# Kernel optimization log

Measured on AMD Instinct MI355X. Metric: run time of the kernel, lower is better.

The kernel has to match this reference:

```python
import jax, jax.numpy as jnp
import numpy as np

B, L, D = 4, 256, 1024
D4 = D // 4
K = 3          # conv kernel size
NL = 3         # num conv layers
MAXLEN = 500   # relative-encoding max_len
R = 8          # rel_types


def _make_pe():
    # sinusoidal table over positions max_len .. -max_len (torch buffer 'pe')
    position = MAXLEN - np.arange(2 * MAXLEN + 1)
    div = np.exp(np.arange(0, D, 2) * (-np.log(10000.0) / D))
    vals = position[:, None] * div[None, :]
    pe = np.zeros((2 * MAXLEN + 1, D), dtype=np.float32)
    pe[:, 0::2] = np.sin(vals)
    pe[:, 1::2] = np.cos(vals)
    return jnp.asarray(pe)

PE = _make_pe()  # constant buffer, (2*max_len+1, D)


def _ln(x, eps=1e-5):
    mu = x.mean(-1, keepdims=True)
    v = ((x - mu) ** 2).mean(-1, keepdims=True)
    return (x - mu) * jax.lax.rsqrt(v + eps)


def setup_inputs() -> dict:
    key = jax.random.key(0)
    ks = jax.random.split(key, 16)
    X = jax.random.normal(ks[0], (B, L, D), jnp.float32)
    lengths = jax.random.randint(ks[1], (B,), L // 2, L + 1)
    mask = jnp.arange(L)[None, :] < lengths[:, None]  # True = valid token
    s = lambda fan: 1.0 / np.sqrt(fan)
    conv_w = jax.random.normal(ks[2], (NL, D, D, K), jnp.float32) * s(D * K)
    conv_b = jnp.zeros((NL, D), jnp.float32)
    Wc = jax.random.normal(ks[3], (D4, D), jnp.float32) * s(D)
    bc = jnp.zeros((D4,), jnp.float32)
    Wp = jax.random.normal(ks[4], (D4, D), jnp.float32) * s(D)
    bp = jnp.zeros((D4,), jnp.float32)
    Wcum = jax.random.normal(ks[5], (D4, D), jnp.float32) * s(D)
    bcum = jnp.zeros((D4,), jnp.float32)
    Wr = jax.random.normal(ks[6], (D4, D), jnp.float32) * s(D)
    br = jnp.zeros((D4,), jnp.float32)
    ln_g = jnp.ones((D4,), jnp.float32)
    ln_b = jnp.zeros((D4,), jnp.float32)
    Wo = jax.random.normal(ks[7], (R, D4), jnp.float32) * 0.05  # zeros at init; use small random for a nontrivial baseline
    bo = jnp.zeros((R,), jnp.float32)
    return {"X": X, "conv_w": conv_w, "conv_b": conv_b, "Wc": Wc, "bc": bc,
            "Wp": Wp, "bp": bp, "Wcum": Wcum, "bcum": bcum, "Wr": Wr, "br": br,
            "ln_g": ln_g, "ln_b": ln_b, "Wo": Wo, "bo": bo, "mask": mask}


def reference(X, conv_w, conv_b, Wc, bc, Wp, bp, Wcum, bcum, Wr, br,
              ln_g, ln_b, Wo, bo, mask):
    vis = mask[:, :, None] & mask[:, None, :]  # (B,L,L)

    # cumulative projection of the raw input (computed before the conv stack)
    cum = jnp.einsum('bld,kd->blk', X, Wcum) + bcum            # (B,L,D4)
    cum = jnp.where(mask[..., None], 0.0, cum)                 # masked_fill(mask, 0) as in source
    cumul_h = jnp.pad(jnp.cumsum(cum, axis=1), ((0, 0), (1, 0), (0, 0)))  # (B,L+1,D4)
    f_cumul = cumul_h[:, :-1]                                   # (B,L,D4)
    b_cumul = cumul_h[:, -1:, :] - cumul_h[:, 1:]               # (B,L,D4)
    cumul_lin = f_cumul[:, :, None, :] - b_cumul[:, None, :, :]  # (B,L,L,D4)

    # conv sequence processor (eval mode: dropout = identity)
    h = X
    for i in range(NL):
        h_in = jnp.where(mask[..., None], h, 0.0)
        xc = jnp.transpose(h_in, (0, 2, 1))                     # (B,D,L)
        yc = jax.lax.conv_general_dilated(
            xc, conv_w[i], window_strides=(1,), padding=[(1, 1)],
            dimension_numbers=('NCH', 'OIH', 'NCH'))
        y = jnp.transpose(yc, (0, 2, 1)) + conv_b[i]            # (B,L,D)
        h = jnp.tanh(_ln(y))                                     # LayerNorm (no affine) + Tanh

    c_lin = h @ Wc.T + bc                                        # (B,L,D4)
    p_lin = h @ Wp.T + bp                                        # (B,L,D4)

    # relative positional scores: relpos[i,j] = transform(pe[max_len + i - j])
    pos = PE @ Wr.T + br                                         # (2*max_len+1, D4)
    idx = MAXLEN + jnp.arange(L)[:, None] - jnp.arange(L)[None, :]
    relpos = pos[idx]                                            # (L,L,D4)

    hid = c_lin[:, :, None, :] + p_lin[:, None, :, :] + cumul_lin + relpos[None]
    hid = jnp.tanh(_ln(hid) * ln_g + ln_b)                       # LayerNorm(affine) + Tanh

    logits = jnp.tanh((hid @ Wo.T + bo) / 7.5) * 7.5             # (B,L,L,R)
    logits = jnp.where(vis[..., None], logits, -64.0)
    root = jnp.transpose(jnp.diagonal(logits, axis1=1, axis2=2), (0, 2, 1))  # (B,L,R)
    return logits, root, h
```

## Files before the change

### kernel.cpp

```cpp
#include <hip/hip_runtime.h>

#define B_ 4
#define L_ 256
#define D_ 1024
#define D4_ 256
#define R_ 8

typedef __attribute__((ext_vector_type(8))) __bf16 bf16x8;
typedef __attribute__((ext_vector_type(4))) __bf16 bf16x4;
typedef __attribute__((ext_vector_type(4))) float f32x4;
typedef __attribute__((ext_vector_type(2))) float f32x2;

__device__ __forceinline__ float4 ld4(const float* p){ return *reinterpret_cast<const float4*>(p); }
__device__ __forceinline__ void st4(float* p, float4 v){ *reinterpret_cast<float4*>(p) = v; }

__device__ __forceinline__ float fast_tanh(float x){
  x = fminf(fmaxf(x, -9.f), 9.f);
  float e = exp2f(x * 2.885390081777927f);
  return (e - 1.f) * __builtin_amdgcn_rcpf(e + 1.f);
}

__device__ __forceinline__ f32x2 fast_tanh2(f32x2 x){
  const f32x2 kk = {2.885390081777927f, 2.885390081777927f};
  f32x2 kx = x * kk;
  float c0 = fminf(fmaxf(kx[0], -26.f), 26.f);
  float c1 = fminf(fmaxf(kx[1], -26.f), 26.f);
  f32x2 e = { exp2f(c0), exp2f(c1) };
  f32x2 den = e + (f32x2){1.f, 1.f};
  f32x2 r = { __builtin_amdgcn_rcpf(den[0]), __builtin_amdgcn_rcpf(den[1]) };
  return (f32x2){-2.f, -2.f} * r + (f32x2){1.f, 1.f};
}

__device__ __forceinline__ int mask_stride(const unsigned char* mask){
  const unsigned int* w = (const unsigned int*)mask;
  unsigned int w0 = w[0];
  if (w0 == 0x01010101u) return 1;
  if (w0 == 0x3F803F80u) return 2;
  if (w0 == 0x3C003C00u) return 2;
  if (w0 == 0x3F800000u) return 4;
  if (w0 == 1u) return (w[1] == 1u) ? 4 : 8;
  if (w0 == 0u && w[1] == 0x3FF00000u) return 8;
  return 1;
}
__device__ __forceinline__ bool mask_at(const unsigned char* mask, int stride, int idx){
  const unsigned char* e = mask + (size_t)idx * stride;
  unsigned char nz = 0;
  for (int s = 0; s < stride; s++) nz |= e[s];
  return nz != 0;
}

__global__ __launch_bounds__(256) void k_megaprep(
    const float* __restrict__ X, const unsigned char* __restrict__ mask,
    __bf16* __restrict__ xu, __bf16* __restrict__ xm,
    const float* __restrict__ cw, __bf16* __restrict__ wbc,
    const float* __restrict__ w0, const float* __restrict__ w1,
    const float* __restrict__ w2, const float* __restrict__ w3,
    __bf16* __restrict__ o0, __bf16* __restrict__ o1,
    __bf16* __restrict__ o2, __bf16* __restrict__ o3,
    __bf16* __restrict__ pe,
    const float* __restrict__ Wo, float* __restrict__ wot)
{
  int blk = blockIdx.x, tid = threadIdx.x;
  if (blk < 512){
    int idx = blk*256 + tid;
    int row = idx >> 7, c8 = (idx & 127) << 3;
    int stride = mask_stride(mask);
    bool keep = mask_at(mask, stride, row);
    const float* src = X + ((size_t)row << 10) + c8;
    bf16x8 u, m;
    #pragma unroll
    for (int e = 0; e < 8; e++){
      float f = src[e];
      u[e] = (__bf16)f;
      m[e] = keep ? (__bf16)f : (__bf16)0.f;
    }
    *reinterpret_cast<bf16x8*>(xu + ((size_t)row<<10) + c8) = u;
    *reinterpret_cast<bf16x8*>(xm + ((size_t)row<<10) + c8) = m;
  } else if (blk < 1024){
    int sub = blk - 512;
    const float* src; __bf16* dst;
    switch (sub >> 7){
      case 0: src = w0; dst = o0; break;
      case 1: src = w1; dst = o1; break;
      case 2: src = w2; dst = o2; break;
      default: src = w3; dst = o3; break;
    }
    int idx = (sub & 127)*256 + tid;
    const float* p = src + (size_t)idx*8;
    bf16x8 v;
    #pragma unroll
    for (int e = 0; e < 8; e++) v[e] = (__bf16)p[e];
    *reinterpret_cast<bf16x8*>(dst + (size_t)idx*8) = v;
  } else if (blk < 4096){
    int idx = (blk - 1024)*256 + tid;
    int layer = idx / 262144;
    int rem = idx & 262143;
    int o = rem >> 8, c4 = (rem & 255) << 2;
    const float* src = cw + (((size_t)layer*1024 + o)*1024 + c4)*3;
    float4 f0 = ld4(src), f1 = ld4(src+4), f2 = ld4(src+8);
    float tv[3][4] = {
      {f0.x, f0.w, f1.z, f2.y},
      {f0.y, f1.x, f1.w, f2.z},
      {f0.z, f1.y, f2.x, f2.w}
    };
    #pragma unroll
    for (int t = 0; t < 3; t++){
      bf16x4 v;
      #pragma unroll
      for (int e = 0; e < 4; e++) v[e] = (__bf16)tv[t][e];
      *reinterpret_cast<bf16x4*>(wbc + ((size_t)(layer*3+t)*1024 + o)*1024 + c4) = v;
    }
  } else if (blk < 4607){
    int t = blk - 4096;
    float posv = (float)(255 - t);
    const float c = -9.210340371976184f / (float)D_;
    for (int m = tid; m < D_/2; m += 256){
      float div = __expf((float)(2*m) * c);
      float val = posv * div;
      pe[((size_t)t<<10) + 2*m]     = (__bf16)__sinf(val);
      pe[((size_t)t<<10) + 2*m + 1] = (__bf16)__cosf(val);
    }
  } else {
    for (int e = tid; e < 2048; e += 256)
      wot[e] = Wo[(((e >> 1) & 7) << 8) + ((e >> 4) << 1) + (e & 1)];
  }
}

__device__ __forceinline__ void gemm_body(__bf16 (*As)[64], __bf16 (*Bs)[64],
                                          const __bf16* __restrict__ A,
                                          const __bf16* __restrict__ Bw,
                                          const float* __restrict__ bias,
                                          const float* __restrict__ bias2,
                                          float* __restrict__ C,
                                          float* __restrict__ Ct,
                                          int M, int N, int Kd,
                                          int row0, int col0, int tid)
{
  int lane = tid & 63, wave = tid >> 6;
  int wv = __builtin_amdgcn_readfirstlane(wave);
  int wm = (wave >> 1) << 5, wn = (wave & 1) << 5;
  __bf16* as_flat = &As[0][0];
  __bf16* bs_flat = &Bs[0][0];
  bool safeA = (row0 + 64 <= M);
  f32x4 acc[2][2] = {};
  for (int k0 = 0; k0 < Kd; k0 += 64){
    if (safeA){
      #pragma unroll
      for (int it = 0; it < 2; it++){
        int sbase = (wv*2 + it) << 6;
        int s = sbase + lane;
        int r = s >> 3, cs = s & 7;
        const __bf16* gp = A + (size_t)(row0 + r)*Kd + k0 + ((cs ^ (r & 7)) << 3);
        __builtin_amdgcn_global_load_lds(gp, as_flat + ((size_t)sbase << 3), 16, 0, 0);
      }
    } else {
      for (int idx = tid; idx < 512; idx += 256){
        int r = idx >> 3, c = idx & 7;
        int row = row0 + r;
        bf16x8 v = {};
        if (row < M) v = *reinterpret_cast<const bf16x8*>(A + (size_t)row*Kd + k0 + (c<<3));
        *reinterpret_cast<bf16x8*>(&As[r][(c ^ (r & 7)) << 3]) = v;
      }
    }
    #pragma unroll
    for (int it = 0; it < 2; it++){
      int sbase = (wv*2 + it) << 6;
      int s = sbase + lane;
      int r = s >> 3, cs = s & 7;
      const __bf16* gp = Bw + (size_t)(col0 + r)*Kd + k0 + ((cs ^ (r & 7)) << 3);
      __builtin_amdgcn_global_load_lds(gp, bs_flat + ((size_t)sbase << 3), 16, 0, 0);
    }
    __syncthreads();
    #pragma unroll
    for (int kk = 0; kk < 2; kk++){
      int kc = (kk << 2) + (lane >> 4);
      int ra0 = wm + (lane & 15), ra1 = ra0 + 16;
      int rb0 = wn + (lane & 15), rb1 = rb0 + 16;
      bf16x8 a0 = *reinterpret_cast<const bf16x8*>(&As[ra0][(kc ^ (ra0 & 7)) << 3]);
      bf16x8 a1 = *reinterpret_cast<const bf16x8*>(&As[ra1][(kc ^ (ra1 & 7)) << 3]);
      bf16x8 b0 = *reinterpret_cast<const bf16x8*>(&Bs[rb0][(kc ^ (rb0 & 7)) << 3]);
      bf16x8 b1 = *reinterpret_cast<const bf16x8*>(&Bs[rb1][(kc ^ (rb1 & 7)) << 3]);
      acc[0][0] = __builtin_amdgcn_mfma_f32_16x16x32_bf16(a0, b0, acc[0][0], 0, 0, 0);
      acc[0][1] = __builtin_amdgcn_mfma_f32_16x16x32_bf16(a0, b1, acc[0][1], 0, 0, 0);
      acc[1][0] = __builtin_amdgcn_mfma_f32_16x16x32_bf16(a1, b0, acc[1][0], 0, 0, 0);
      acc[1][1] = __builtin_amdgcn_mfma_f32_16x16x32_bf16(a1, b1, acc[1][1], 0, 0, 0);
    }
    __syncthreads();
  }
  #pragma unroll
  for (int mi = 0; mi < 2; mi++)
    #pragma unroll
    for (int ni = 0; ni < 2; ni++){
      int col = col0 + wn + (ni << 4) + (lane & 15);
      float bv = bias ? ((col < 256) ? bias[col] : bias2[col - 256]) : 0.f;
      int rowb = row0 + wm + (mi << 4) + ((lane >> 4) << 2);
      if (Ct){
        float* dst = Ct + ((size_t)(col >> 2) << 11) + (col & 3);
        #pragma unroll
        for (int e = 0; e < 4; e++){
          int row = rowb + e;
          if (row < M) dst[row << 2] = acc[mi][ni][e] + bv;
        }
      } else {
        #pragma unroll
        for (int e = 0; e < 4; e++){
          int row = rowb + e;
          if (row < M) C[(size_t)row*N + col] = acc[mi][ni][e] + bv;
        }
      }
    }
}

__global__ __launch_bounds__(256) void k_gemm3(
    const __bf16* __restrict__ Xb_u, const __bf16* __restrict__ Wcum_b,
    const float* __restrict__ bcum, float* __restrict__ cum,
    const __bf16* __restrict__ hb_fin, const __bf16* __restrict__ Wc_b,
    const float* __restrict__ bc, const float* __restrict__ bp,
    float* __restrict__ cp_lin,
    const __bf16* __restrict__ pe_b, const __bf16* __restrict__ Wr_b,
    const float* __restrict__ br, float* __restrict__ pos_t)
{
  __shared__ __align__(16) __bf16 As[64][64];
  __shared__ __align__(16) __bf16 Bs[64][64];
  int blk = blockIdx.x, tid = threadIdx.x;
  if (blk < 64){
    gemm_body(As, Bs, Xb_u, Wcum_b, bcum, bcum, cum, nullptr,
              1024, 256, 1024, (blk & 15) << 6, (blk >> 4) << 6, tid);
  } else if (blk < 192){
    int s = blk - 64;
    gemm_body(As, Bs, hb_fin, Wc_b, bc, bp, cp_lin, nullptr,
              1024, 512, 1024, (s & 15) << 6, (s >> 4) << 6, tid);
  } else {
    int s = blk - 192;
    gemm_body(As, Bs, pe_b, Wr_b, br, br, nullptr, pos_t,
              511, 256, 1024, (s & 7) << 6, (s >> 3) << 6, tid);
  }
}

__global__ __launch_bounds__(256) void k_gemm_cross(
    const __bf16* __restrict__ ci_bf, const __bf16* __restrict__ pj_bf,
    const __bf16* __restrict__ pos_bf,
    float* __restrict__ G1, float* __restrict__ G2, float* __restrict__ G3)
{
  __shared__ __align__(16) __bf16 As[64][64];
  __shared__ __align__(16) __bf16 Bs[64][64];
  int blk = blockIdx.x, tid = threadIdx.x;
  if (blk < 64){
    int b = blk >> 4, s = blk & 15;
    gemm_body(As, Bs, ci_bf + ((size_t)b << 16), pj_bf + ((size_t)b << 16),
              nullptr, nullptr, G1 + ((size_t)b << 16), nullptr,
              256, 256, 256, (s & 3) << 6, (s >> 2) << 6, tid);
  } else if (blk < 192){
    int s = blk - 64;
    gemm_body(As, Bs, ci_bf, pos_bf, nullptr, nullptr, G2, nullptr,
              1024, 512, 256, (s & 15) << 6, (s >> 4) << 6, tid);
  } else {
    int s = blk - 192;
    gemm_body(As, Bs, pj_bf, pos_bf, nullptr, nullptr, G3, nullptr,
              1024, 512, 256, (s & 15) << 6, (s >> 4) << 6, tid);
  }
}

__global__ __launch_bounds__(256) void k_conv_mfma(const __bf16* __restrict__ hb,
                                                   const __bf16* __restrict__ wbc,
                                                   __bf16* __restrict__ y, int layer)
{
  __shared__ __align__(16) __bf16 As[66][64];
  __shared__ __align__(16) __bf16 Bs[3][64][64];
  int tid = threadIdx.x;
  int lane = tid & 63, wave = tid >> 6;
  int wv = __builtin_amdgcn_readfirstlane(wave);
  int wm = (wave >> 1) << 5, wn = (wave & 1) << 5;
  int n = blockIdx.x;
  int swz = (n & 7)*128 + (n >> 3);
  int bx = swz & 15, oy = (swz >> 4) & 15, z = swz >> 8;
  int b = bx >> 2, l0 = (bx & 3) << 6;
  int o0 = oy << 6;
  __bf16* as_flat = &As[0][0];
  __bf16* bs_flat = &Bs[0][0][0];
  f32x4 acc[2][2] = {};
  for (int cc = 0; cc < 4; cc++){
    int c0 = (z << 8) + (cc << 6);
    #pragma unroll
    for (int it = 0; it < 6; it++){
      int m = wv*6 + it;
      int s = (m << 6) + lane;
      int t = s >> 9, r = (s >> 3) & 63, c_ = s & 7;
      const __bf16* gp = wbc + ((size_t)((layer*3 + t) << 10) + o0 + r)*1024
                       + c0 + ((c_ ^ (r & 7)) << 3);
      __builtin_amdgcn_global_load_lds(gp, bs_flat + ((size_t)m << 9), 16, 0, 0);
    }
    #pragma unroll
    for (int it = 0; it < 2; it++){
      int sbase = (wv*2 + it) << 6;
      int s = sbase + lane;
      int r = 1 + (s >> 3), c = s & 7;
      const __bf16* gp = hb + (((size_t)(b<<8) + l0 - 1 + r) << 10)
                       + c0 + ((c ^ (r & 7)) << 3);
      __builtin_amdgcn_global_load_lds(gp, as_flat + 64 + ((size_t)sbase << 3), 16, 0, 0);
    }
    if (tid < 16){
      int rr = (tid >> 3) ? 65 : 0;
      int c = tid & 7;
      int l = l0 - 1 + rr;
      bf16x8 v = {};
      if (l >= 0 && l < L_)
        v = *reinterpret_cast<const bf16x8*>(hb + (((size_t)(b<<8) + l) << 10) + c0 + (c<<3));
      *reinterpret_cast<bf16x8*>(&As[rr][(c ^ (rr & 7)) << 3]) = v;
    }
    __syncthreads();
    #pragma unroll
    for (int t = 0; t < 3; t++){
      #pragma unroll
      for (int kk = 0; kk < 2; kk++){
        int kc = (kk << 2) + (lane >> 4);
        int ra0 = wm + (lane & 15) + t, ra1 = ra0 + 16;
        int rb0 = wn + (lane & 15),     rb1 = rb0 + 16;
        bf16x8 a0 = *reinterpret_cast<const bf16x8*>(&As[ra0][(kc ^ (ra0 & 7)) << 3]);
        bf16x8 a1 = *reinterpret_cast<const bf16x8*>(&As[ra1][(kc ^ (ra1 & 7)) << 3]);
        bf16x8 b0 = *reinterpret_cast<const bf16x8*>(&Bs[t][rb0][(kc ^ (rb0 & 7)) << 3]);
        bf16x8 b1 = *reinterpret_cast<const bf16x8*>(&Bs[t][rb1][(kc ^ (rb1 & 7)) << 3]);
        acc[0][0] = __builtin_amdgcn_mfma_f32_16x16x32_bf16(a0, b0, acc[0][0], 0, 0, 0);
        acc[0][1] = __builtin_amdgcn_mfma_f32_16x16x32_bf16(a0, b1, acc[0][1], 0, 0, 0);
        acc[1][0] = __builtin_amdgcn_mfma_f32_16x16x32_bf16(a1, b0, acc[1][0], 0, 0, 0);
        acc[1][1] = __builtin_amdgcn_mfma_f32_16x16x32_bf16(a1, b1, acc[1][1], 0, 0, 0);
      }
    }
    __syncthreads();
  }
  __bf16* yz = y + (size_t)z * 1048576;
  #pragma unroll
  for (int mi = 0; mi < 2; mi++)
    #pragma unroll
    for (int ni = 0; ni < 2; ni++){
      int col = o0 + wn + (ni << 4) + (lane & 15);
      #pragma unroll
      for (int e = 0; e < 4; e++){
        int rowl = wm + (mi << 4) + ((lane >> 4) << 2) + e;
        yz[(((size_t)(b<<8) + l0 + rowl) << 10) + col] = (__bf16)acc[mi][ni][e];
      }
    }
}

__device__ __forceinline__ void ln_core4(const __bf16* y, const float* cb, int n, int tid,
                                         int lane, int wid, float* red,
                                         float4& v, float& mu, float& rstd){
  const __bf16* yr = y + ((size_t)n << 10) + tid*4;
  bf16x4 a0 = *reinterpret_cast<const bf16x4*>(yr);
  bf16x4 a1 = *reinterpret_cast<const bf16x4*>(yr + 1048576);
  bf16x4 a2 = *reinterpret_cast<const bf16x4*>(yr + 2097152);
  bf16x4 a3 = *reinterpret_cast<const bf16x4*>(yr + 3145728);
  float4 bb = ld4(cb + tid*4);
  v = make_float4((float)a0[0]+(float)a1[0]+(float)a2[0]+(float)a3[0]+bb.x,
                  (float)a0[1]+(float)a1[1]+(float)a2[1]+(float)a3[1]+bb.y,
                  (float)a0[2]+(float)a1[2]+(float)a2[2]+(float)a3[2]+bb.z,
                  (float)a0[3]+(float)a1[3]+(float)a2[3]+(float)a3[3]+bb.w);
  float s = v.x+v.y+v.z+v.w;
  #pragma unroll
  for (int m=1;m<64;m<<=1) s += __shfl_xor(s, m);
  if (lane == 0) red[wid] = s;
  __syncthreads();
  mu = (red[0]+red[1]+red[2]+red[3]) * (1.f/D_);
  float d0=v.x-mu, d1=v.y-mu, d2=v.z-mu, d3=v.w-mu;
  float ss = d0*d0+d1*d1+d2*d2+d3*d3;
  #pragma unroll
  for (int m=1;m<64;m<<=1) ss += __shfl_xor(ss, m);
  if (lane == 0) red[8+wid] = ss;
  __syncthreads();
  rstd = rsqrtf((red[8]+red[9]+red[10]+red[11]) * (1.f/D_) + 1e-5f);
}

__global__ __launch_bounds__(256) void k_ln_tanh_mid(const __bf16* __restrict__ y,
                                                     const float* __restrict__ cb,
                                                     const unsigned char* __restrict__ mask,
                                                     __bf16* __restrict__ hb)
{
  __shared__ float red[16];
  int n = blockIdx.x;
  int tid = threadIdx.x, lane = tid & 63, wid = tid >> 6;
  float4 v; float mu, rstd;
  ln_core4(y, cb, n, tid, lane, wid, red, v, mu, rstd);
  int stride = mask_stride(mask);
  float keep = mask_at(mask, stride, n) ? 1.f : 0.f;
  bf16x4 o;
  o[0] = (__bf16)(fast_tanh((v.x-mu)*rstd) * keep);
  o[1] = (__bf16)(fast_tanh((v.y-mu)*rstd) * keep);
  o[2] = (__bf16)(fast_tanh((v.z-mu)*rstd) * keep);
  o[3] = (__bf16)(fast_tanh((v.w-mu)*rstd) * keep);
  *reinterpret_cast<bf16x4*>(hb + ((size_t)n<<10) + tid*4) = o;
}

__global__ __launch_bounds__(256) void k_ln_tanh_fin(const __bf16* __restrict__ y,
                                                     const float* __restrict__ cb,
                                                     float* __restrict__ hf,
                                                     __bf16* __restrict__ hb)
{
  __shared__ float red[16];
  int n = blockIdx.x;
  int tid = threadIdx.x, lane = tid & 63, wid = tid >> 6;
  float4 v; float mu, rstd;
  ln_core4(y, cb, n, tid, lane, wid, red, v, mu, rstd);
  float t0 = fast_tanh((v.x-mu)*rstd), t1 = fast_tanh((v.y-mu)*rstd);
  float t2 = fast_tanh((v.z-mu)*rstd), t3 = fast_tanh((v.w-mu)*rstd);
  st4(&hf[((size_t)n<<10) + tid*4], make_float4(t0,t1,t2,t3));
  bf16x4 o; o[0]=(__bf16)t0; o[1]=(__bf16)t1; o[2]=(__bf16)t2; o[3]=(__bf16)t3;
  *reinterpret_cast<bf16x4*>(hb + ((size_t)n<<10) + tid*4) = o;
}

__global__ __launch_bounds__(256) void k_combine(const float* __restrict__ cum,
                                                 const float* __restrict__ cp,
                                                 const unsigned char* __restrict__ mask,
                                                 float* __restrict__ ci,
                                                 float* __restrict__ pjt)
{
  __shared__ unsigned char mflag[256];
  int tid = threadIdx.x;
  int b = blockIdx.x >> 6;
  {
    int stride = mask_stride(mask);
    mflag[tid] = mask_at(mask, stride, (b << 8) + tid) ? 1 : 0;
  }
  __syncthreads();
  int w = blockIdx.x*4 + (tid >> 6);
  int lane = tid & 63;
  int k = w & 255;
  int rowbase = b << 8;
  float v[4], p[4];
  float run = 0.f;
  #pragma unroll
  for (int e = 0; e < 4; e++){
    int l = lane*4 + e;
    float x = cum[(((size_t)rowbase + l) << 8) + k];
    v[e] = mflag[l] ? 0.f : x;
    run += v[e]; p[e] = run;
  }
  float t = run, s = run;
  #pragma unroll
  for (int off = 1; off < 64; off <<= 1){
    float u = __shfl_up(s, off);
    if (lane >= off) s += u;
  }
  float excl = s - t;
  float total = __shfl(s, 63);
  float* pjb = pjt + (((size_t)((k >> 2)*4 + b)) << 10) + (k & 3);
  #pragma unroll
  for (int e = 0; e < 4; e++){
    int l = lane*4 + e;
    size_t row = rowbase + l;
    float f_ex = excl + p[e] - v[e];
    float b_in = total - (excl + p[e]);
    ci[(row << 8) + k] = cp[row*512 + k] + f_ex;
    pjb[l << 2] = cp[row*512 + 256 + k] - b_in;
  }
}

__global__ __launch_bounds__(256) void k_rowstats(const float* __restrict__ ci,
                                                  const float* __restrict__ pjt,
                                                  const float* __restrict__ post,
                                                  __bf16* __restrict__ ci_bf,
                                                  __bf16* __restrict__ pj_bf,
                                                  __bf16* __restrict__ pos_bf,
                                                  float* __restrict__ stats)
{
  int w = blockIdx.x*4 + (threadIdx.x >> 6);
  int lane = threadIdx.x & 63;
  float4 v; __bf16* dst; float* Sp; float* Qp;
  if (w < 1024){
    v = ld4(&ci[((size_t)w << 8) + (lane << 2)]);
    dst = ci_bf + ((size_t)w << 8) + (lane << 2);
    Sp = stats + w; Qp = stats + 1024 + w;
  } else if (w < 2048){
    int row = w - 1024;
    int b = row >> 8, j = row & 255;
    v = ld4(pjt + ((size_t)lane << 12) + (b << 10) + (j << 2));
    dst = pj_bf + ((size_t)row << 8) + (lane << 2);
    Sp = stats + 2048 + row; Qp = stats + 3072 + row;
  } else {
    int d = w - 2048;
    if (d < 511) v = ld4(post + ((size_t)lane << 11) + (d << 2));
    else         v = make_float4(0.f, 0.f, 0.f, 0.f);
    dst = pos_bf + ((size_t)d << 8) + (lane << 2);
    Sp = stats + 4096 + d; Qp = stats + 4608 + d;
  }
  bf16x4 o; o[0]=(__bf16)v.x; o[1]=(__bf16)v.y; o[2]=(__bf16)v.z; o[3]=(__bf16)v.w;
  *reinterpret_cast<bf16x4*>(dst) = o;
  float s = v.x+v.y+v.z+v.w;
  float qv = v.x*v.x + v.y*v.y + v.z*v.z + v.w*v.w;
  #pragma unroll
  for (int m = 1; m < 64; m <<= 1){
    s  += __shfl_xor(s,  m);
    qv += __shfl_xor(qv, m);
  }
  if (lane == 0){ *Sp = s; *Qp = qv; }
}

__global__ __launch_bounds__(256) void k_pairs(const float* __restrict__ ci,
                                               const float* __restrict__ pjt,
                                               const float* __restrict__ post,
                                               const float* __restrict__ ln_g,
                                               const float* __restrict__ ln_b,
                                               const float* __restrict__ wot,
                                               const float* __restrict__ bo,
                                               const unsigned char* __restrict__ mask,
                                               const float* __restrict__ stats,
                                               const float* __restrict__ G1,
                                               const float* __restrict__ G2,
                                               const float* __restrict__ G3,
                                               float* __restrict__ out)
{
  __shared__ float pacc[64][3][9];

  int bid = blockIdx.x;
  int qtr = bid & 3;
  int bi = bid >> 2;
  int b = bi >> 8, i = bi & 255;
  int tid = threadIdx.x;
  int jj = tid & 63, q = tid >> 6;
  int j = (qtr << 6) + jj;

  int d = i - j + 255;
  int bj = (b << 8) + j;
  const float* pjb = pjt + ((size_t)b << 10) + (j << 2);
  const float* pob = post + ((size_t)d << 2);
  const float* cbase = ci + ((size_t)bi << 8);
  int k40 = __builtin_amdgcn_readfirstlane(q << 4);

  float Sh = stats[bi] + stats[2048 + bj] + stats[4096 + d];
  float Qh = stats[1024 + bi] + stats[3072 + bj] + stats[4608 + d]
           + 2.f*(G1[((size_t)b << 16) + (i << 8) + j]
                + G2[((size_t)bi << 9) + d]
                + G3[((size_t)bj << 9) + d]);
  float mu = Sh * (1.f/256.f);
  float var = fmaxf(Qh * (1.f/256.f) - mu*mu, 0.f);
  float rstd = rsqrtf(var + 1e-5f);

  f32x2 aP0={0,0},aP1={0,0},aP2={0,0},aP3={0,0},aP4={0,0},aP5={0,0},aP6={0,0},aP7={0,0};
  f32x2 mmu = {-mu, -mu}, rr = {rstd, rstd};
  #pragma unroll 4
  for (int u = 0; u < 16; u++){
    int k4 = k40 + u;
    float4 c4 = ld4(cbase + (k4 << 2));
    float4 g4 = ld4(ln_g + (k4 << 2));
    float4 b4 = ld4(ln_b + (k4 << 2));
    float4 pv = ld4(pjb + ((size_t)k4 << 12));
    float4 ov = ld4(pob + ((size_t)k4 << 11));
    const float* wf = wot + (k4 << 5);
    float4 w0 = ld4(wf),      w1 = ld4(wf + 4);
    float4 w2 = ld4(wf + 8),  w3 = ld4(wf + 12);
    float4 w4 = ld4(wf + 16), w5 = ld4(wf + 20);
    float4 w6 = ld4(wf + 24), w7 = ld4(wf + 28);
    f32x2 hA = (f32x2){c4.x, c4.y} + (f32x2){pv.x, pv.y} + (f32x2){ov.x, ov.y};
    f32x2 hB = (f32x2){c4.z, c4.w} + (f32x2){pv.z, pv.w} + (f32x2){ov.z, ov.w};
    f32x2 gA = {g4.x, g4.y}, gB = {g4.z, g4.w};
    f32x2 bA = {b4.x, b4.y}, bB = {b4.z, b4.w};
    f32x2 argA = ((hA + mmu) * rr) * gA + bA;
    f32x2 argB = ((hB + mmu) * rr) * gB + bB;
    f32x2 vA = fast_tanh2(argA);
    f32x2 vB = fast_tanh2(argB);
    aP0 = vA * (f32x2){w0.x, w0.y} + aP0;  aP1 = vA * (f32x2){w0.z, w0.w} + aP1;
    aP2 = vA * (f32x2){w1.x, w1.y} + aP2;  aP3 = vA * (f32x2){w1.z, w1.w} + aP3;
    aP4 = vA * (f32x2){w2.x, w2.y} + aP4;  aP5 = vA * (f32x2){w2.z, w2.w} + aP5;
    aP6 = vA * (f32x2){w3.x, w3.y} + aP6;  aP7 = vA * (f32x2){w3.z, w3.w} + aP7;
    aP0 = vB * (f32x2){w4.x, w4.y} + aP0;  aP1 = vB * (f32x2){w4.z, w4.w} + aP1;
    aP2 = vB * (f32x2){w5.x, w5.y} + aP2;  aP3 = vB * (f32x2){w5.z, w5.w} + aP3;
    aP4 = vB * (f32x2){w6.x, w6.y} + aP4;  aP5 = vB * (f32x2){w6.z, w6.w} + aP5;
    aP6 = vB * (f32x2){w7.x, w7.y} + aP6;  aP7 = vB * (f32x2){w7.z, w7.w} + aP7;
  }
  float a0 = aP0[0]+aP0[1], a1 = aP1[0]+aP1[1];
  float a2 = aP2[0]+aP2[1], a3 = aP3[0]+aP3[1];
  float a4 = aP4[0]+aP4[1], a5 = aP5[0]+aP5[1];
  float a6 = aP6[0]+aP6[1], a7 = aP7[0]+aP7[1];
  if (q){
    float* pp = &pacc[jj][q-1][0];
    pp[0]=a0; pp[1]=a1; pp[2]=a2; pp[3]=a3;
    pp[4]=a4; pp[5]=a5; pp[6]=a6; pp[7]=a7;
  }
  __syncthreads();
  if (!q){
    const float* p0 = &pacc[jj][0][0];
    const float* p1 = &pacc[jj][1][0];
    const float* p2 = &pacc[jj][2][0];
    a0 += p0[0]+p1[0]+p2[0]; a1 += p0[1]+p1[1]+p2[1];
    a2 += p0[2]+p1[2]+p2[2]; a3 += p0[3]+p1[3]+p2[3];
    a4 += p0[4]+p1[4]+p2[4]; a5 += p0[5]+p1[5]+p2[5];
    a6 += p0[6]+p1[6]+p2[6]; a7 += p0[7]+p1[7]+p2[7];
    float acc[8] = {a0,a1,a2,a3,a4,a5,a6,a7};
    int stride = mask_stride(mask);
    bool vis = mask_at(mask, stride, bi) && mask_at(mask, stride, bj);
    float res[8];
    #pragma unroll
    for (int r = 0; r < 8; r++){
      float sc = (acc[r] + bo[r]) * (1.f/7.5f);
      res[r] = vis ? fast_tanh(sc)*7.5f : -64.f;
    }
    float* lp = out + (((size_t)bi << 8) + j)*8;
    st4(lp,     make_float4(res[0],res[1],res[2],res[3]));
    st4(lp + 4, make_float4(res[4],res[5],res[6],res[7]));
    if (j == i){
      float* rp = out + (size_t)B_*L_*L_*R_ + ((size_t)bi)*8;
      st4(rp,     make_float4(res[0],res[1],res[2],res[3]));
      st4(rp + 4, make_float4(res[4],res[5],res[6],res[7]));
    }
  }
}

extern "C" void kernel_launch(void* const* d_in, const int* in_sizes, int n_in,
                              void* d_out, int out_size, void* d_ws, size_t ws_size,
                              hipStream_t stream)
{
  const float* X      = (const float*)d_in[0];
  const float* conv_w = (const float*)d_in[1];
  const float* conv_b = (const float*)d_in[2];
  const float* Wc     = (const float*)d_in[3];
  const float* bc     = (const float*)d_in[4];
  const float* Wp     = (const float*)d_in[5];
  const float* bp     = (const float*)d_in[6];
  const float* Wcum   = (const float*)d_in[7];
  const float* bcum   = (const float*)d_in[8];
  const float* Wr     = (const float*)d_in[9];
  const float* br     = (const float*)d_in[10];
  const float* ln_g   = (const float*)d_in[11];
  const float* ln_b   = (const float*)d_in[12];
  const float* Wo     = (const float*)d_in[13];
  const float* bo     = (const float*)d_in[14];
  const unsigned char* mask = (const unsigned char*)d_in[15];
  float* out = (float*)d_out;

  char* base = (char*)d_ws;
  auto alloc = [&](size_t bytes){ char* p = base; base += (bytes + 255) & ~(size_t)255; return p; };
  __bf16* Xb_u    = (__bf16*)alloc(2097152);
  __bf16* Xb_m    = (__bf16*)alloc(2097152);
  __bf16* Wbc     = (__bf16*)alloc(18874368);
  __bf16* Wcum_b  = (__bf16*)alloc(524288);
  __bf16* Wc_b    = (__bf16*)alloc(524288);
  __bf16* Wp_b    = (__bf16*)alloc(524288);
  __bf16* Wr_b    = (__bf16*)alloc(524288);
  __bf16* pe_b    = (__bf16*)alloc(1046528);
  __bf16* ypart   = (__bf16*)alloc(8388608);
  __bf16* hb_mid  = (__bf16*)alloc(2097152);
  __bf16* hb_fin  = (__bf16*)alloc(2097152);
  float*  cum     = (float*) alloc(1048576);
  float*  cp_lin  = (float*) alloc(2097152);
  float*  ci_c    = (float*) alloc(1048576);
  float*  pj_t    = (float*) alloc(1048576);
  float*  pos_t   = (float*) alloc(524288);
  __bf16* ci_bf   = (__bf16*)alloc(524288);
  __bf16* pj_bf   = (__bf16*)alloc(524288);
  __bf16* pos_bf  = (__bf16*)alloc(262144);
  float*  statsB  = (float*) alloc(20480);
  float*  G1      = (float*) alloc(1048576);
  float*  G2      = (float*) alloc(2097152);
  float*  G3      = (float*) alloc(2097152);
  float*  wot     = (float*) alloc(8192);
  (void)Wp_b;

  float* h_out = out + (size_t)B_*L_*L_*R_ + (size_t)B_*L_*R_;

  k_megaprep<<<4608, 256, 0, stream>>>(X, mask, Xb_u, Xb_m, conv_w, Wbc,
                                       Wcum, Wc, Wp, Wr, Wcum_b, Wc_b, Wp_b, Wr_b,
                                       pe_b, Wo, wot);

  k_conv_mfma<<<1024, 256, 0, stream>>>(Xb_m,   Wbc, ypart, 0);
  k_ln_tanh_mid<<<B_*L_, 256, 0, stream>>>(ypart, conv_b,        mask, hb_mid);
  k_conv_mfma<<<1024, 256, 0, stream>>>(hb_mid, Wbc, ypart, 1);
  k_ln_tanh_mid<<<B_*L_, 256, 0, stream>>>(ypart, conv_b + 1024, mask, hb_mid);
  k_conv_mfma<<<1024, 256, 0, stream>>>(hb_mid, Wbc, ypart, 2);
  k_ln_tanh_fin<<<B_*L_, 256, 0, stream>>>(ypart, conv_b + 2048, h_out, hb_fin);

  k_gemm3<<<224, 256, 0, stream>>>(Xb_u, Wcum_b, bcum, cum,
                                   hb_fin, Wc_b, bc, bp, cp_lin,
                                   pe_b, Wr_b, br, pos_t);

  k_combine<<<256, 256, 0, stream>>>(cum, cp_lin, mask, ci_c, pj_t);

  k_rowstats<<<640, 256, 0, stream>>>(ci_c, pj_t, pos_t, ci_bf, pj_bf, pos_bf, statsB);
  k_gemm_cross<<<320, 256, 0, stream>>>(ci_bf, pj_bf, pos_bf, G1, G2, G3);

  k_pairs<<<B_*L_*4, 256, 0, stream>>>(ci_c, pj_t, pos_t, ln_g, ln_b, wot, bo,
                                       mask, statsB, G1, G2, G3, out);
}
```

Baseline: 148.2 us.

## Compute pair-hidden to logits projection with bf16 MFMA via LDS-staged tanh values

In k_pairs, each thread previously ran a scalar FMA projection of its tanh-activated hidden vector onto the 8 output weights, followed by an LDS reduction across four waves. Now the tanh outputs are packed to bf16 into a swizzled LDS tile (64 pairs by 256 features), and each wave runs 16x16x32 bf16 MFMAs against a zero-padded 16-row bf16 copy of Wo. This moves the dot products onto matrix cores and removes the partial-sum reduction. In exchange the activations and weights lose precision to bf16, half of the MFMA columns are padding, and the output stores become scalar per element.

After: 157.2 us. +6.1%, slower.

```diff
diff --git a/kernel.cpp b/kernel.cpp
--- a/kernel.cpp
+++ b/kernel.cpp
@@ -29,6 +29,13 @@
   f32x2 den = e + (f32x2){1.f, 1.f};
   f32x2 r = { __builtin_amdgcn_rcpf(den[0]), __builtin_amdgcn_rcpf(den[1]) };
   return (f32x2){-2.f, -2.f} * r + (f32x2){1.f, 1.f};
+}
+
+__device__ __forceinline__ unsigned pack_bf16(float a, float b){
+  __bf16 x = (__bf16)a, y = (__bf16)b;
+  unsigned short ux = __builtin_bit_cast(unsigned short, x);
+  unsigned short uy = __builtin_bit_cast(unsigned short, y);
+  return (unsigned)ux | ((unsigned)uy << 16);
 }
 
 __device__ __forceinline__ int mask_stride(const unsigned char* mask){
@@ -58,7 +65,7 @@
     __bf16* __restrict__ o0, __bf16* __restrict__ o1,
     __bf16* __restrict__ o2, __bf16* __restrict__ o3,
     __bf16* __restrict__ pe,
-    const float* __restrict__ Wo, float* __restrict__ wot)
+    const float* __restrict__ Wo, __bf16* __restrict__ wot16)
 {
   int blk = blockIdx.x, tid = threadIdx.x;
   if (blk < 512){
@@ -121,8 +128,10 @@
       pe[((size_t)t<<10) + 2*m + 1] = (__bf16)__cosf(val);
     }
   } else {
-    for (int e = tid; e < 2048; e += 256)
-      wot[e] = Wo[(((e >> 1) & 7) << 8) + ((e >> 4) << 1) + (e & 1)];
+    for (int e = tid; e < 4096; e += 256){
+      int r = e >> 8, k = e & 255;
+      wot16[e] = (r < 8) ? (__bf16)Wo[(r << 8) + k] : (__bf16)0.f;
+    }
   }
 }
 
@@ -499,7 +508,7 @@
                                                const float* __restrict__ post,
                                                const float* __restrict__ ln_g,
                                                const float* __restrict__ ln_b,
-                                               const float* __restrict__ wot,
+                                               const __bf16* __restrict__ wot16,
                                                const float* __restrict__ bo,
                                                const unsigned char* __restrict__ mask,
                                                const float* __restrict__ stats,
@@ -508,7 +517,7 @@
                                                const float* __restrict__ G3,
                                                float* __restrict__ out)
 {
-  __shared__ float pacc[64][3][9];
+  __shared__ __align__(16) __bf16 V[64][256];
 
   int bid = blockIdx.x;
   int qtr = bid & 3;
@@ -534,72 +543,63 @@
   float var = fmaxf(Qh * (1.f/256.f) - mu*mu, 0.f);
   float rstd = rsqrtf(var + 1e-5f);
 
-  f32x2 aP0={0,0},aP1={0,0},aP2={0,0},aP3={0,0},aP4={0,0},aP5={0,0},aP6={0,0},aP7={0,0};
   f32x2 mmu = {-mu, -mu}, rr = {rstd, rstd};
-  #pragma unroll 4
-  for (int u = 0; u < 16; u++){
-    int k4 = k40 + u;
-    float4 c4 = ld4(cbase + (k4 << 2));
-    float4 g4 = ld4(ln_g + (k4 << 2));
-    float4 b4 = ld4(ln_b + (k4 << 2));
-    float4 pv = ld4(pjb + ((size_t)k4 << 12));
-    float4 ov = ld4(pob + ((size_t)k4 << 11));
-    const float* wf = wot + (k4 << 5);
-    float4 w0 = ld4(wf),      w1 = ld4(wf + 4);
-    float4 w2 = ld4(wf + 8),  w3 = ld4(wf + 12);
-    float4 w4 = ld4(wf + 16), w5 = ld4(wf + 20);
-    float4 w6 = ld4(wf + 24), w7 = ld4(wf + 28);
-    f32x2 hA = (f32x2){c4.x, c4.y} + (f32x2){pv.x, pv.y} + (f32x2){ov.x, ov.y};
-    f32x2 hB = (f32x2){c4.z, c4.w} + (f32x2){pv.z, pv.w} + (f32x2){ov.z, ov.w};
-    f32x2 gA = {g4.x, g4.y}, gB = {g4.z, g4.w};
-    f32x2 bA = {b4.x, b4.y}, bB = {b4.z, b4.w};
-    f32x2 argA = ((hA + mmu) * rr) * gA + bA;
-    f32x2 argB = ((hB + mmu) * rr) * gB + bB;
-    f32x2 vA = fast_tanh2(argA);
-    f32x2 vB = fast_tanh2(argB);
-    aP0 = vA * (f32x2){w0.x, w0.y} + aP0;  aP1 = vA * (f32x2){w0.z, w0.w} + aP1;
-    aP2 = vA * (f32x2){w1.x, w1.y} + aP2;  aP3 = vA * (f32x2){w1.z, w1.w} + aP3;
-    aP4 = vA * (f32x2){w2.x, w2.y} + aP4;  aP5 = vA * (f32x2){w2.z, w2.w} + aP5;
-    aP6 = vA * (f32x2){w3.x, w3.y} + aP6;  aP7 = vA * (f32x2){w3.z, w3.w} + aP7;
-    aP0 = vB * (f32x2){w4.x, w4.y} + aP0;  aP1 = vB * (f32x2){w4.z, w4.w} + aP1;
-    aP2 = vB * (f32x2){w5.x, w5.y} + aP2;  aP3 = vB * (f32x2){w5.z, w5.w} + aP3;
-    aP4 = vB * (f32x2){w6.x, w6.y} + aP4;  aP5 = vB * (f32x2){w6.z, w6.w} + aP5;
-    aP6 = vB * (f32x2){w7.x, w7.y} + aP6;  aP7 = vB * (f32x2){w7.z, w7.w} + aP7;
-  }
-  float a0 = aP0[0]+aP0[1], a1 = aP1[0]+aP1[1];
-  float a2 = aP2[0]+aP2[1], a3 = aP3[0]+aP3[1];
-  float a4 = aP4[0]+aP4[1], a5 = aP5[0]+aP5[1];
-  float a6 = aP6[0]+aP6[1], a7 = aP7[0]+aP7[1];
-  if (q){
-    float* pp = &pacc[jj][q-1][0];
-    pp[0]=a0; pp[1]=a1; pp[2]=a2; pp[3]=a3;
-    pp[4]=a4; pp[5]=a5; pp[6]=a6; pp[7]=a7;
+  #pragma unroll
+  for (int uu = 0; uu < 8; uu++){
+    unsigned pk[4];
+    #pragma unroll
+    for (int h2 = 0; h2 < 2; h2++){
+      int k4 = k40 + 2*uu + h2;
+      float4 c4 = ld4(cbase + (k4 << 2));
+      float4 g4 = ld4(ln_g + (k4 << 2));
+      float4 b4 = ld4(ln_b + (k4 << 2));
+      float4 pv = ld4(pjb + ((size_t)k4 << 12));
+      float4 ov = ld4(pob + ((size_t)k4 << 11));
+      f32x2 hA = (f32x2){c4.x, c4.y} + (f32x2){pv.x, pv.y} + (f32x2){ov.x, ov.y};
+      f32x2 hB = (f32x2){c4.z, c4.w} + (f32x2){pv.z, pv.w} + (f32x2){ov.z, ov.w};
+      f32x2 gA = {g4.x, g4.y}, gB = {g4.z, g4.w};
+      f32x2 bA = {b4.x, b4.y}, bB = {b4.z, b4.w};
+      f32x2 vA = fast_tanh2(((hA + mmu) * rr) * gA + bA);
+      f32x2 vB = fast_tanh2(((hB + mmu) * rr) * gB + bB);
+      pk[2*h2]   = pack_bf16(vA[0], vA[1]);
+      pk[2*h2+1] = pack_bf16(vB[0], vB[1]);
+    }
+    int c = (q << 3) + uu;
+    uint4 wv = {pk[0], pk[1], pk[2], pk[3]};
+    *reinterpret_cast<uint4*>(&V[jj][(c ^ (jj & 7)) << 3]) = wv;
   }
   __syncthreads();
-  if (!q){
-    const float* p0 = &pacc[jj][0][0];
-    const float* p1 = &pacc[jj][1][0];
-    const float* p2 = &pacc[jj][2][0];
-    a0 += p0[0]+p1[0]+p2[0]; a1 += p0[1]+p1[1]+p2[1];
-    a2 += p0[2]+p1[2]+p2[2]; a3 += p0[3]+p1[3]+p2[3];
-    a4 += p0[4]+p1[4]+p2[4]; a5 += p0[5]+p1[5]+p2[5];
-    a6 += p0[6]+p1[6]+p2[6]; a7 += p0[7]+p1[7]+p2[7];
-    float acc[8] = {a0,a1,a2,a3,a4,a5,a6,a7};
+
+  bf16x8 bfr[8];
+  #pragma unroll
+  for (int s = 0; s < 8; s++){
+    int kc = (s << 2) + (jj >> 4);
+    bfr[s] = *reinterpret_cast<const bf16x8*>(wot16 + ((jj & 15) << 8) + (kc << 3));
+  }
+  f32x4 acc = {};
+  #pragma unroll
+  for (int s = 0; s < 8; s++){
+    int kc = (s << 2) + (jj >> 4);
+    int row = (q << 4) + (jj & 15);
+    bf16x8 av = *reinterpret_cast<const bf16x8*>(&V[row][(kc ^ (row & 7)) << 3]);
+    acc = __builtin_amdgcn_mfma_f32_16x16x32_bf16(av, bfr[s], acc, 0, 0, 0);
+  }
+
+  int r = jj & 15;
+  if (r < 8){
     int stride = mask_stride(mask);
-    bool vis = mask_at(mask, stride, bi) && mask_at(mask, stride, bj);
-    float res[8];
-    #pragma unroll
-    for (int r = 0; r < 8; r++){
-      float sc = (acc[r] + bo[r]) * (1.f/7.5f);
-      res[r] = vis ? fast_tanh(sc)*7.5f : -64.f;
-    }
-    float* lp = out + (((size_t)bi << 8) + j)*8;
-    st4(lp,     make_float4(res[0],res[1],res[2],res[3]));
-    st4(lp + 4, make_float4(res[4],res[5],res[6],res[7]));
-    if (j == i){
-      float* rp = out + (size_t)B_*L_*L_*R_ + ((size_t)bi)*8;
-      st4(rp,     make_float4(res[0],res[1],res[2],res[3]));
-      st4(rp + 4, make_float4(res[4],res[5],res[6],res[7]));
+    bool visi = mask_at(mask, stride, bi);
+    float bor = bo[r];
+    #pragma unroll
+    for (int e = 0; e < 4; e++){
+      int jl = (q << 4) + ((jj >> 4) << 2) + e;
+      int jg = (qtr << 6) + jl;
+      bool vis = visi && mask_at(mask, stride, (b << 8) + jg);
+      float sc = (acc[e] + bor) * (1.f/7.5f);
+      float res = vis ? fast_tanh(sc)*7.5f : -64.f;
+      out[(((size_t)bi << 8) + jg)*8 + r] = res;
+      if (jg == i)
+        out[(size_t)B_*L_*L_*R_ + ((size_t)bi)*8 + r] = res;
     }
   }
 }
@@ -651,14 +651,14 @@
   float*  G1      = (float*) alloc(1048576);
   float*  G2      = (float*) alloc(2097152);
   float*  G3      = (float*) alloc(2097152);
-  float*  wot     = (float*) alloc(8192);
+  __bf16* wot16   = (__bf16*)alloc(8192);
   (void)Wp_b;
 
   float* h_out = out + (size_t)B_*L_*L_*R_ + (size_t)B_*L_*R_;
 
   k_megaprep<<<4608, 256, 0, stream>>>(X, mask, Xb_u, Xb_m, conv_w, Wbc,
                                        Wcum, Wc, Wp, Wr, Wcum_b, Wc_b, Wp_b, Wr_b,
-                                       pe_b, Wo, wot);
+                                       pe_b, Wo, wot16);
 
   k_conv_mfma<<<1024, 256, 0, stream>>>(Xb_m,   Wbc, ypart, 0);
   k_ln_tanh_mid<<<B_*L_, 256, 0, stream>>>(ypart, conv_b,        mask, hb_mid);
@@ -676,6 +676,6 @@
   k_rowstats<<<640, 256, 0, stream>>>(ci_c, pj_t, pos_t, ci_bf, pj_bf, pos_bf, statsB);
   k_gemm_cross<<<320, 256, 0, stream>>>(ci_bf, pj_bf, pos_bf, G1, G2, G3);
 
-  k_pairs<<<B_*L_*4, 256, 0, stream>>>(ci_c, pj_t, pos_t, ln_g, ln_b, wot, bo,
+  k_pairs<<<B_*L_*4, 256, 0, stream>>>(ci_c, pj_t, pos_t, ln_g, ln_b, wot16, bo,
                                        mask, statsB, G1, G2, G3, out);
 }
```
